# Kernel tuning notes

Measured on AMD Instinct MI355X. Metric: run time of the kernel, lower is better.

Reference implementation:

```python
import jax, jax.numpy as jnp
import numpy as np

TAU_MIN, TAU_MAX, TAU_SMALL, N_REF = 0.005, 0.1, 0.3, 4


def _l2norm(x, eps=1e-12):
    # matches torch F.normalize: x / max(||x||_2, eps)
    n = jnp.linalg.norm(x, axis=-1, keepdims=True)
    return x / jnp.maximum(n, eps)


def setup_inputs() -> dict:
    key = jax.random.key(0)
    k1, k2, k3 = jax.random.split(key, 3)
    B, C, H, W = 8, 384, 40, 40
    feats = jax.random.normal(k1, (B, C, H, W), dtype=jnp.float32)
    refs = jax.random.normal(k2, (N_REF, B, C, H, W), dtype=jnp.float32)
    sopm = jax.random.uniform(k3, (B, 1, 160, 160), dtype=jnp.float32)
    log_tau = jnp.array([np.log(0.03)], dtype=jnp.float32)
    alpha_raw = jnp.array([0.0], dtype=jnp.float32)
    return {"feats": feats, "refs": refs, "sopm": sopm,
            "log_tau": log_tau, "alpha_raw": alpha_raw}


def reference(feats, refs, sopm, log_tau, alpha_raw):
    B, C, H, W = feats.shape
    N = H * W
    # buffer contents and SOPM cache are detached in the torch module
    refs = jax.lax.stop_gradient(refs)
    sopm = jax.lax.stop_gradient(sopm)

    tau = jnp.clip(jnp.exp(log_tau[0]), TAU_MIN, TAU_MAX)
    alpha = jax.nn.sigmoid(alpha_raw[0])

    tokens = feats.reshape(B, C, N).transpose(0, 2, 1)   # [B, N, C]
    cur_n = _l2norm(tokens)

    n_ref = refs.shape[0]
    warped_sum = jnp.zeros_like(tokens)
    for r in range(n_ref):  # fixed small ref-frame loop (n_ref=4)
        ref_tok = refs[r].reshape(B, C, N).transpose(0, 2, 1)  # [B, N, C]
        ref_n = _l2norm(ref_tok)
        sim = jnp.einsum('bnc,bmc->bnm', cur_n, ref_n)          # cosine sims
        w = jax.nn.softmax(sim / tau, axis=-1)                  # [B, N, N]
        warped_sum = warped_sum + jnp.einsum('bnm,bmc->bnc', w, ref_tok)
    warped = warped_sum / n_ref

    # SOPM(t-1) -> bilinear resize (align_corners=False) -> threshold mask
    sopm_r = jax.image.resize(sopm, (B, 1, H, W), method='bilinear')
    mask = (sopm_r.reshape(B, 1, N).transpose(0, 2, 1) > TAU_SMALL).astype(feats.dtype)  # [B,N,1]

    alpha_eff = alpha  # full buffer: n_avail == n_ref
    fused = alpha_eff * warped + (1.0 - alpha_eff) * tokens
    enhanced = mask * fused + (1.0 - mask) * tokens
    return enhanced.transpose(0, 2, 1).reshape(B, C, H, W)
```

## Files before the change

### kernel.cpp

```cpp
#include <hip/hip_runtime.h>
#include <stdint.h>

#define B_  8
#define C_  384
#define N_  1600
#define R_  4
#define S_  160
#define HW_ 40

typedef float  f32x4  __attribute__((ext_vector_type(4)));
typedef __bf16 bf16x8 __attribute__((ext_vector_type(8)));
typedef long long i64t;

__device__ __forceinline__ unsigned short f2bf(float x){
  __bf16 h = (__bf16)x;
  return __builtin_bit_cast(unsigned short, h);
}
__device__ __forceinline__ float bf2f(unsigned short u){
  return __builtin_bit_cast(float, (uint32_t)u << 16);
}
__device__ __forceinline__ uint32_t pk_fp8x4(float a, float b, float c, float d){
  int lo = __builtin_amdgcn_cvt_pk_fp8_f32(a, b, 0, false);
  int hi = __builtin_amdgcn_cvt_pk_fp8_f32(c, d, 0, false);
  return (uint32_t)(lo & 0xffff) | ((uint32_t)hi << 16);
}

__device__ __forceinline__ void gload_lds16(const void* g, void* l){
  __builtin_amdgcn_global_load_lds(
      (const __attribute__((address_space(1))) uint32_t*)g,
      (__attribute__((address_space(3))) uint32_t*)l, 16, 0, 0);
}

__global__ void norm_kernel(const float* __restrict__ feats,
                            const float* __restrict__ refs,
                            float* __restrict__ invn){
  int gid = blockIdx.x * 256 + threadIdx.x;
  if (gid >= 16000) return;
  int mat = gid / 400;
  int n4  = (gid - mat * 400) * 4;
  const float* src = (mat < B_) ? (feats + (size_t)mat * C_ * N_)
                                : (refs  + (size_t)(mat - B_) * C_ * N_);
  f32x4 ss = {0.f,0.f,0.f,0.f};
  for (int c = 0; c < C_; ++c){
    f32x4 v = *(const f32x4*)(src + (size_t)c * N_ + n4);
    ss += v * v;
  }
  f32x4 r;
#pragma unroll
  for (int i = 0; i < 4; ++i) r[i] = 1.f / fmaxf(sqrtf(ss[i]), 1e-12f);
  *(f32x4*)(invn + (size_t)mat * N_ + n4) = r;
}

__global__ void prep_kernel(const float* __restrict__ feats,
                            const float* __restrict__ refs,
                            const float* __restrict__ invn,
                            unsigned char* __restrict__ Qb,
                            unsigned char* __restrict__ Kb,
                            unsigned short* __restrict__ Vb){
  int nt = blockIdx.x, ct = blockIdx.y, mat = blockIdx.z;
  __shared__ float tile[64][65];
  int t = threadIdx.x;
  bool isref = (mat >= B_);
  const float* src = isref ? refs  + (size_t)(mat - B_) * C_ * N_
                           : feats + (size_t)mat * C_ * N_;
#pragma unroll
  for (int i = 0; i < 4; ++i){
    int chunk = t + 256 * i;
    int cr = chunk >> 4, n4 = chunk & 15;
    size_t off = (size_t)(ct * 64 + cr) * N_ + nt * 64 + n4 * 4;
    float4 v = *(const float4*)(src + off);
    tile[cr][n4 * 4 + 0] = v.x;  tile[cr][n4 * 4 + 1] = v.y;
    tile[cr][n4 * 4 + 2] = v.z;  tile[cr][n4 * 4 + 3] = v.w;
    if (isref){
      ushort4 o;
      o.x = f2bf(v.x); o.y = f2bf(v.y); o.z = f2bf(v.z); o.w = f2bf(v.w);
      unsigned short* vdst = Vb + (size_t)(mat - B_) * C_ * N_;
      *(ushort4*)(vdst + off) = o;
    }
  }
  __syncthreads();
  unsigned char* dst = isref ? Kb + (size_t)(mat - B_) * N_ * C_
                             : Qb + (size_t)mat * N_ * C_;
  const float* ivp = invn + (size_t)mat * N_ + nt * 64;
#pragma unroll
  for (int i = 0; i < 4; ++i){
    int chunk = t + 256 * i;
    int nr = chunk >> 4, c4 = chunk & 15;
    float iv = ivp[nr];
    uint32_t pk = pk_fp8x4(tile[c4*4+0][nr] * iv, tile[c4*4+1][nr] * iv,
                           tile[c4*4+2][nr] * iv, tile[c4*4+3][nr] * iv);
    *(uint32_t*)(dst + (size_t)(nt*64+nr) * C_ + ct*64 + c4*4) = pk;
  }
}

__global__ void mask_kernel(const float* __restrict__ sopm,
                            float* __restrict__ maskp){
  int gid = blockIdx.x * 256 + threadIdx.x;
  int b = gid / N_, n = gid - b * N_;
  int oy = n / HW_, ox = n - oy * HW_;
  const float* sp = sopm + (size_t)b * S_ * S_;
  float cy = oy * 4 + 1.5f, cx = ox * 4 + 1.5f;
  int y0 = 4*oy - 2; if (y0 < 0) y0 = 0;
  int y1 = 4*oy + 5; if (y1 > S_-1) y1 = S_-1;
  int x0 = 4*ox - 2; if (x0 < 0) x0 = 0;
  int x1 = 4*ox + 5; if (x1 > S_-1) x1 = S_-1;
  float wsy = 0.f, wsx = 0.f;
  for (int j = y0; j <= y1; ++j) wsy += 1.f - fabsf(j - cy) * 0.25f;
  for (int j = x0; j <= x1; ++j) wsx += 1.f - fabsf(j - cx) * 0.25f;
  float acc = 0.f;
  for (int jy = y0; jy <= y1; ++jy){
    float wy = 1.f - fabsf(jy - cy) * 0.25f;
    float rs = 0.f;
    for (int jx = x0; jx <= x1; ++jx)
      rs += (1.f - fabsf(jx - cx) * 0.25f) * sp[jy * S_ + jx];
    acc += wy * rs;
  }
  float val = acc / (wsy * wsx);
  maskp[gid] = (val > 0.3f) ? 1.f : 0.f;
}

#define KB0_   0
#define KB1_   12288
#define VB_    24576
#define P_OFF  49152
#define LDS_SZ 53248

__global__ __launch_bounds__(256, 2) void attn_kernel(
    const unsigned char* __restrict__ Qb,
    const unsigned char* __restrict__ Kb,
    const unsigned short* __restrict__ Vb,
    const float* __restrict__ log_tau,
    unsigned short* __restrict__ Or)
{
  __shared__ __align__(16) char lds[LDS_SZ];
  int wg   = blockIdx.x;
  int orig = (wg & 7) * 100 + (wg >> 3);
  int qt   = orig % 25;
  int rb   = orig / 25;
  int b    = rb & 7;
  int tid  = threadIdx.x;
  int lane = tid & 63;
  int w    = tid >> 6;
  int mw   = w >> 1;
  int qw   = w & 1;
  int l15  = lane & 15;
  int lg   = lane >> 4;

  float tau = expf(log_tau[0]);
  tau = fminf(fmaxf(tau, 0.005f), 0.1f);
  float sc = 1.4426950408889634f / tau;

  i64t qreg[2][12];
#pragma unroll
  for (int qt2 = 0; qt2 < 2; ++qt2){
    const unsigned char* qp = Qb +
        ((size_t)b * N_ + qt * 64 + qw * 32 + qt2 * 16 + l15) * C_ + lg * 8;
#pragma unroll
    for (int ks = 0; ks < 12; ++ks)
      qreg[qt2][ks] = *(const i64t*)(qp + ks * 32);
  }

  f32x4 o[4][6];
#pragma unroll
  for (int i = 0; i < 4; ++i)
#pragma unroll
    for (int j = 0; j < 6; ++j) o[i][j] = (f32x4){0.f,0.f,0.f,0.f};
  float lsum0 = 0.f, lsum1 = 0.f;

  const unsigned char*  kmat = Kb + (size_t)rb * N_ * C_;
  const unsigned short* vmat = Vb + (size_t)rb * C_ * N_;
  char* Pb = lds + P_OFF;

  int koffB[3];
#pragma unroll
  for (int i = 0; i < 3; ++i){
    int L = (w * 3 + i) * 64 + lane;
    int m   = L / 24;
    int pos = L - m * 24;
    int cc  = (pos >> 3) * 8 + ((pos & 7) ^ (m & 7));
    koffB[i] = m * C_ + cc * 16;
  }
  int voff[6];
#pragma unroll
  for (int i = 0; i < 6; ++i){
    int chunk = (w * 6 + i) * 64 + lane;
    int line = chunk >> 3;
    int u    = (chunk & 7) ^ (line & 7);
    voff[i]  = (line * 2 + (u >> 2)) * N_ + (u & 3) * 8;
  }

  const int s_l  = (l15 >> 1) & 3;
  const int p_w0 = (qw*32      + l15) * 64 + (((2*mw + (lg >> 1)) ^ s_l) << 4) + (lg & 1) * 8;
  const int p_w1 = (qw*32 + 16 + l15) * 64 + (((2*mw + (lg >> 1)) ^ s_l) << 4) + (lg & 1) * 8;
  const int p_rc = ((lg ^ s_l) << 4) + l15 * 64;

  auto stageK = [&](int t, int buf){
    const unsigned char* kb = kmat + (size_t)t * 32 * C_;
    char* kdst = lds + (buf ? KB1_ : KB0_) + w * 3072;
#pragma unroll
    for (int i = 0; i < 3; ++i) gload_lds16(kb + koffB[i], kdst + i * 1024);
  };
  auto stageV = [&](int t){
    const unsigned short* vb = vmat + t * 32;
    char* vdst = lds + VB_ + w * 6144;
#pragma unroll
    for (int i = 0; i < 6; ++i) gload_lds16(vb + voff[i], vdst + i * 1024);
  };

  stageK(0, 0);
  stageV(0);
  stageK(1, 1);
  asm volatile("s_waitcnt vmcnt(9)" ::: "memory");
  __builtin_amdgcn_sched_barrier(0);
  __builtin_amdgcn_s_barrier();
  __builtin_amdgcn_sched_barrier(0);

  const int krow = (mw * 16 + l15);
  for (int mt = 0; mt < 50; ++mt){
    int cur = mt & 1;
    const char* kbR = lds + (cur ? KB1_ : KB0_);

    f32x4 s0 = {0.f,0.f,0.f,0.f}, s1 = {0.f,0.f,0.f,0.f};
    __builtin_amdgcn_s_setprio(1);
#pragma unroll
    for (int ks = 0; ks < 12; ++ks){
      int lc  = 2 * ks + (lg >> 1);
      int off = ((lc >> 3) * 8 + ((lc & 7) ^ (krow & 7))) * 16 + (lg & 1) * 8;
      i64t a = *(const i64t*)(kbR + krow * 384 + off);
      s0 = __builtin_amdgcn_mfma_f32_16x16x32_fp8_fp8(a, qreg[0][ks], s0, 0, 0, 0);
      s1 = __builtin_amdgcn_mfma_f32_16x16x32_fp8_fp8(a, qreg[1][ks], s1, 0, 0, 0);
    }
    __builtin_amdgcn_s_setprio(0);

    ushort4 pw0, pw1;
    {
      __bf16 h;
      float l0 = 0.f, l1 = 0.f;
      h = (__bf16)exp2f((s0[0]-1.f)*sc); l0 += (float)h; pw0.x = __builtin_bit_cast(unsigned short, h);
      h = (__bf16)exp2f((s0[1]-1.f)*sc); l0 += (float)h; pw0.y = __builtin_bit_cast(unsigned short, h);
      h = (__bf16)exp2f((s0[2]-1.f)*sc); l0 += (float)h; pw0.z = __builtin_bit_cast(unsigned short, h);
      h = (__bf16)exp2f((s0[3]-1.f)*sc); l0 += (float)h; pw0.w = __builtin_bit_cast(unsigned short, h);
      h = (__bf16)exp2f((s1[0]-1.f)*sc); l1 += (float)h; pw1.x = __builtin_bit_cast(unsigned short, h);
      h = (__bf16)exp2f((s1[1]-1.f)*sc); l1 += (float)h; pw1.y = __builtin_bit_cast(unsigned short, h);
      h = (__bf16)exp2f((s1[2]-1.f)*sc); l1 += (float)h; pw1.z = __builtin_bit_cast(unsigned short, h);
      h = (__bf16)exp2f((s1[3]-1.f)*sc); l1 += (float)h; pw1.w = __builtin_bit_cast(unsigned short, h);
      lsum0 += l0; lsum1 += l1;
    }
    *(ushort4*)(Pb + p_w0) = pw0;
    *(ushort4*)(Pb + p_w1) = pw1;
    asm volatile("s_waitcnt lgkmcnt(0) vmcnt(0)" ::: "memory");
    __builtin_amdgcn_sched_barrier(0);
    __builtin_amdgcn_s_barrier();
    __builtin_amdgcn_sched_barrier(0);

    int tk = (mt + 2 < 50) ? mt + 2 : mt;
    stageK(tk, cur);
    __builtin_amdgcn_sched_barrier(0);

    bf16x8 pa[4];
#pragma unroll
    for (int qf2 = 0; qf2 < 4; ++qf2)
      pa[qf2] = *(const bf16x8*)(Pb + qf2 * 1024 + p_rc);
    __builtin_amdgcn_s_setprio(1);
#pragma unroll
    for (int cf = 0; cf < 6; ++cf){
      int c  = w * 96 + cf * 16 + l15;
      int vo = (c >> 1) * 128 + (((lg | ((c & 1) << 2)) ^ ((c >> 1) & 7)) << 4);
      bf16x8 vf = *(const bf16x8*)(lds + VB_ + vo);
#pragma unroll
      for (int qf2 = 0; qf2 < 4; ++qf2)
        o[qf2][cf] = __builtin_amdgcn_mfma_f32_16x16x32_bf16(pa[qf2], vf, o[qf2][cf], 0, 0, 0);
    }
    __builtin_amdgcn_s_setprio(0);

    __builtin_amdgcn_sched_barrier(0);
    __builtin_amdgcn_s_barrier();
    __builtin_amdgcn_sched_barrier(0);

    int tv = (mt + 1 < 50) ? mt + 1 : 49;
    stageV(tv);
    __builtin_amdgcn_sched_barrier(0);
  }

  lsum0 += __shfl_xor(lsum0, 16, 64);
  lsum0 += __shfl_xor(lsum0, 32, 64);
  lsum1 += __shfl_xor(lsum1, 16, 64);
  lsum1 += __shfl_xor(lsum1, 32, 64);
  __syncthreads();
  float* lsh = (float*)lds;
  if (lg == 0){
    lsh[mw * 64 + qw * 32 + l15]      = lsum0;
    lsh[mw * 64 + qw * 32 + 16 + l15] = lsum1;
  }
  __syncthreads();
  float invl[4][4];
#pragma unroll
  for (int qf2 = 0; qf2 < 4; ++qf2)
#pragma unroll
    for (int rg = 0; rg < 4; ++rg){
      int q = qf2 * 16 + lg * 4 + rg;
      invl[qf2][rg] = 1.f / (lsh[q] + lsh[64 + q]);
    }

  int qbase = qt * 64;
  unsigned short* op = Or + ((size_t)rb * N_ + qbase) * C_ + w * 96 + l15;
#pragma unroll
  for (int qf2 = 0; qf2 < 4; ++qf2){
#pragma unroll
    for (int cf = 0; cf < 6; ++cf){
#pragma unroll
      for (int rg = 0; rg < 4; ++rg){
        int q = qf2 * 16 + lg * 4 + rg;
        op[(size_t)q * C_ + cf * 16] = f2bf(o[qf2][cf][rg] * invl[qf2][rg]);
      }
    }
  }
}

__global__ void combine_kernel(const unsigned short* __restrict__ Or,
                               const float* __restrict__ feats,
                               const float* __restrict__ maskp,
                               const float* __restrict__ alpha_raw,
                               float* __restrict__ out){
  int nt = blockIdx.x, ct = blockIdx.y, b = blockIdx.z;
  __shared__ float tile[64][65];
  float alpha = 1.f / (1.f + expf(-alpha_raw[0]));
  int t = threadIdx.x;
#pragma unroll
  for (int i = 0; i < 4; ++i){
    int chunk = t + 256 * i;
    int nr = chunk >> 4, c4 = chunk & 15;
    size_t base = ((size_t)b * N_ + nt * 64 + nr) * C_ + ct * 64 + c4 * 4;
    float4 s = {0.f,0.f,0.f,0.f};
#pragma unroll
    for (int r = 0; r < 4; ++r){
      ushort4 v = *(const ushort4*)(Or + (size_t)r * B_ * N_ * C_ + base);
      s.x += bf2f(v.x); s.y += bf2f(v.y); s.z += bf2f(v.z); s.w += bf2f(v.w);
    }
    tile[nr][c4*4+0] = s.x; tile[nr][c4*4+1] = s.y;
    tile[nr][c4*4+2] = s.z; tile[nr][c4*4+3] = s.w;
  }
  __syncthreads();
#pragma unroll
  for (int i = 0; i < 4; ++i){
    int chunk = t + 256 * i;
    int cr = chunk >> 4, n4 = chunk & 15;
    size_t fb = ((size_t)b * C_ + ct * 64 + cr) * N_ + nt * 64 + n4 * 4;
    float4 f  = *(const float4*)(feats + fb);
    float4 mk = *(const float4*)(maskp + (size_t)b * N_ + nt * 64 + n4 * 4);
    float4 ov;
    ov.x = f.x + mk.x * alpha * (tile[n4*4+0][cr] * 0.25f - f.x);
    ov.y = f.y + mk.y * alpha * (tile[n4*4+1][cr] * 0.25f - f.y);
    ov.z = f.z + mk.z * alpha * (tile[n4*4+2][cr] * 0.25f - f.z);
    ov.w = f.w + mk.w * alpha * (tile[n4*4+3][cr] * 0.25f - f.w);
    *(float4*)(out + fb) = ov;
  }
}

__global__ void poison_kernel(float* out, int n){
  int i = blockIdx.x * 256 + threadIdx.x;
  if (i < n) out[i] = 1.0e6f;
}

extern "C" void kernel_launch(void* const* d_in, const int* in_sizes, int n_in,
                              void* d_out, int out_size, void* d_ws, size_t ws_size,
                              hipStream_t stream){
  const float* feats     = (const float*)d_in[0];
  const float* refs      = (const float*)d_in[1];
  const float* sopm      = (const float*)d_in[2];
  const float* log_tau   = (const float*)d_in[3];
  const float* alpha_raw = (const float*)d_in[4];
  float* out = (float*)d_out;

  const size_t SZ_INVN = (size_t)(1 + R_) * B_ * N_ * 4;
  const size_t SZ_MASK = (size_t)B_ * N_ * 4;
  const size_t SZ_QB   = (size_t)B_ * N_ * C_;
  const size_t SZ_KB   = (size_t)R_ * B_ * N_ * C_;
  const size_t SZ_VB   = (size_t)R_ * B_ * N_ * C_ * 2;
  const size_t SZ_OR   = (size_t)R_ * B_ * N_ * C_ * 2;
  const size_t need = SZ_INVN + SZ_MASK + SZ_QB + SZ_KB + SZ_VB + SZ_OR;

  if (ws_size < need){
    poison_kernel<<<(out_size + 255) / 256, 256, 0, stream>>>(out, out_size);
    return;
  }
  char* ws = (char*)d_ws;
  float*          invn  = (float*)ws;
  float*          maskp = (float*)(ws + SZ_INVN);
  unsigned char*  Qb    = (unsigned char*)(ws + SZ_INVN + SZ_MASK);
  unsigned char*  Kb    = (unsigned char*)(ws + SZ_INVN + SZ_MASK + SZ_QB);
  unsigned short* Vb    = (unsigned short*)(ws + SZ_INVN + SZ_MASK + SZ_QB + SZ_KB);
  unsigned short* Or    = (unsigned short*)(ws + SZ_INVN + SZ_MASK + SZ_QB + SZ_KB + SZ_VB);

  norm_kernel   <<<63, 256, 0, stream>>>(feats, refs, invn);
  mask_kernel   <<<50, 256, 0, stream>>>(sopm, maskp);
  prep_kernel   <<<dim3(25, 6, 40), 256, 0, stream>>>(feats, refs, invn, Qb, Kb, Vb);
  attn_kernel   <<<800, 256, 0, stream>>>(Qb, Kb, Vb, log_tau, Or);
  combine_kernel<<<dim3(25, 6, 8), 256, 0, stream>>>(Or, feats, maskp, alpha_raw, out);
}
```

Before: 222.7 us.

## Split attention workgroup work across eight waves instead of four

Doubles the attention kernel's block size to 512 threads, so each wave handles 16 query rows for QK and 48 output channels for PV instead of 32 rows and 96 channels. The intent is to cut per-wave register pressure (accumulators and Q fragments) and add more waves to hide latency. In exchange, QK MFMA work is split finer with less K-fragment reuse per wave, only half the waves stage K, and the prologue now waits fully before issuing the second K prefetch. More barrier participants per iteration may add sync cost.

```diff
diff --git a/kernel.cpp b/kernel.cpp
--- a/kernel.cpp
+++ b/kernel.cpp
@@ -125,7 +125,7 @@
 #define P_OFF  49152
 #define LDS_SZ 53248
 
-__global__ __launch_bounds__(256, 2) void attn_kernel(
+__global__ __launch_bounds__(512, 2) void attn_kernel(
     const unsigned char* __restrict__ Qb,
     const unsigned char* __restrict__ Kb,
     const unsigned short* __restrict__ Vb,
@@ -141,8 +141,8 @@
   int tid  = threadIdx.x;
   int lane = tid & 63;
   int w    = tid >> 6;
-  int mw   = w >> 1;
-  int qw   = w & 1;
+  int mw   = w >> 2;
+  int qw   = w & 3;
   int l15  = lane & 15;
   int lg   = lane >> 4;
 
@@ -150,22 +150,21 @@
   tau = fminf(fmaxf(tau, 0.005f), 0.1f);
   float sc = 1.4426950408889634f / tau;
 
-  i64t qreg[2][12];
-#pragma unroll
-  for (int qt2 = 0; qt2 < 2; ++qt2){
+  i64t qreg[12];
+  {
     const unsigned char* qp = Qb +
-        ((size_t)b * N_ + qt * 64 + qw * 32 + qt2 * 16 + l15) * C_ + lg * 8;
+        ((size_t)b * N_ + qt * 64 + qw * 16 + l15) * C_ + lg * 8;
 #pragma unroll
     for (int ks = 0; ks < 12; ++ks)
-      qreg[qt2][ks] = *(const i64t*)(qp + ks * 32);
-  }
-
-  f32x4 o[4][6];
+      qreg[ks] = *(const i64t*)(qp + ks * 32);
+  }
+
+  f32x4 o[4][3];
 #pragma unroll
   for (int i = 0; i < 4; ++i)
 #pragma unroll
-    for (int j = 0; j < 6; ++j) o[i][j] = (f32x4){0.f,0.f,0.f,0.f};
-  float lsum0 = 0.f, lsum1 = 0.f;
+    for (int j = 0; j < 3; ++j) o[i][j] = (f32x4){0.f,0.f,0.f,0.f};
+  float lsum = 0.f;
 
   const unsigned char*  kmat = Kb + (size_t)rb * N_ * C_;
   const unsigned short* vmat = Vb + (size_t)rb * C_ * N_;
@@ -174,80 +173,75 @@
   int koffB[3];
 #pragma unroll
   for (int i = 0; i < 3; ++i){
-    int L = (w * 3 + i) * 64 + lane;
+    int L = ((w & 3) * 3 + i) * 64 + lane;
     int m   = L / 24;
     int pos = L - m * 24;
     int cc  = (pos >> 3) * 8 + ((pos & 7) ^ (m & 7));
     koffB[i] = m * C_ + cc * 16;
   }
-  int voff[6];
-#pragma unroll
-  for (int i = 0; i < 6; ++i){
-    int chunk = (w * 6 + i) * 64 + lane;
+  int voff[3];
+#pragma unroll
+  for (int i = 0; i < 3; ++i){
+    int chunk = (w * 3 + i) * 64 + lane;
     int line = chunk >> 3;
     int u    = (chunk & 7) ^ (line & 7);
     voff[i]  = (line * 2 + (u >> 2)) * N_ + (u & 3) * 8;
   }
 
   const int s_l  = (l15 >> 1) & 3;
-  const int p_w0 = (qw*32      + l15) * 64 + (((2*mw + (lg >> 1)) ^ s_l) << 4) + (lg & 1) * 8;
-  const int p_w1 = (qw*32 + 16 + l15) * 64 + (((2*mw + (lg >> 1)) ^ s_l) << 4) + (lg & 1) * 8;
+  const int p_w  = (qw*16 + l15) * 64 + (((mw*2 + (lg >> 1)) ^ s_l) << 4) + (lg & 1) * 8;
   const int p_rc = ((lg ^ s_l) << 4) + l15 * 64;
 
   auto stageK = [&](int t, int buf){
-    const unsigned char* kb = kmat + (size_t)t * 32 * C_;
-    char* kdst = lds + (buf ? KB1_ : KB0_) + w * 3072;
-#pragma unroll
-    for (int i = 0; i < 3; ++i) gload_lds16(kb + koffB[i], kdst + i * 1024);
+    if (w < 4){
+      const unsigned char* kb = kmat + (size_t)t * 32 * C_;
+      char* kdst = lds + (buf ? KB1_ : KB0_) + w * 3072;
+#pragma unroll
+      for (int i = 0; i < 3; ++i) gload_lds16(kb + koffB[i], kdst + i * 1024);
+    }
   };
   auto stageV = [&](int t){
     const unsigned short* vb = vmat + t * 32;
-    char* vdst = lds + VB_ + w * 6144;
-#pragma unroll
-    for (int i = 0; i < 6; ++i) gload_lds16(vb + voff[i], vdst + i * 1024);
+    char* vdst = lds + VB_ + w * 3072;
+#pragma unroll
+    for (int i = 0; i < 3; ++i) gload_lds16(vb + voff[i], vdst + i * 1024);
   };
 
   stageK(0, 0);
   stageV(0);
-  stageK(1, 1);
-  asm volatile("s_waitcnt vmcnt(9)" ::: "memory");
+  asm volatile("s_waitcnt vmcnt(0)" ::: "memory");
   __builtin_amdgcn_sched_barrier(0);
   __builtin_amdgcn_s_barrier();
   __builtin_amdgcn_sched_barrier(0);
+  stageK(1, 1);
 
   const int krow = (mw * 16 + l15);
   for (int mt = 0; mt < 50; ++mt){
     int cur = mt & 1;
     const char* kbR = lds + (cur ? KB1_ : KB0_);
 
-    f32x4 s0 = {0.f,0.f,0.f,0.f}, s1 = {0.f,0.f,0.f,0.f};
+    f32x4 s0 = {0.f,0.f,0.f,0.f};
     __builtin_amdgcn_s_setprio(1);
 #pragma unroll
     for (int ks = 0; ks < 12; ++ks){
       int lc  = 2 * ks + (lg >> 1);
       int off = ((lc >> 3) * 8 + ((lc & 7) ^ (krow & 7))) * 16 + (lg & 1) * 8;
       i64t a = *(const i64t*)(kbR + krow * 384 + off);
-      s0 = __builtin_amdgcn_mfma_f32_16x16x32_fp8_fp8(a, qreg[0][ks], s0, 0, 0, 0);
-      s1 = __builtin_amdgcn_mfma_f32_16x16x32_fp8_fp8(a, qreg[1][ks], s1, 0, 0, 0);
+      s0 = __builtin_amdgcn_mfma_f32_16x16x32_fp8_fp8(a, qreg[ks], s0, 0, 0, 0);
     }
     __builtin_amdgcn_s_setprio(0);
 
-    ushort4 pw0, pw1;
+    ushort4 pw;
     {
       __bf16 h;
-      float l0 = 0.f, l1 = 0.f;
-      h = (__bf16)exp2f((s0[0]-1.f)*sc); l0 += (float)h; pw0.x = __builtin_bit_cast(unsigned short, h);
-      h = (__bf16)exp2f((s0[1]-1.f)*sc); l0 += (float)h; pw0.y = __builtin_bit_cast(unsigned short, h);
-      h = (__bf16)exp2f((s0[2]-1.f)*sc); l0 += (float)h; pw0.z = __builtin_bit_cast(unsigned short, h);
-      h = (__bf16)exp2f((s0[3]-1.f)*sc); l0 += (float)h; pw0.w = __builtin_bit_cast(unsigned short, h);
-      h = (__bf16)exp2f((s1[0]-1.f)*sc); l1 += (float)h; pw1.x = __builtin_bit_cast(unsigned short, h);
-      h = (__bf16)exp2f((s1[1]-1.f)*sc); l1 += (float)h; pw1.y = __builtin_bit_cast(unsigned short, h);
-      h = (__bf16)exp2f((s1[2]-1.f)*sc); l1 += (float)h; pw1.z = __builtin_bit_cast(unsigned short, h);
-      h = (__bf16)exp2f((s1[3]-1.f)*sc); l1 += (float)h; pw1.w = __builtin_bit_cast(unsigned short, h);
-      lsum0 += l0; lsum1 += l1;
-    }
-    *(ushort4*)(Pb + p_w0) = pw0;
-    *(ushort4*)(Pb + p_w1) = pw1;
+      float l0 = 0.f;
+      h = (__bf16)exp2f((s0[0]-1.f)*sc); l0 += (float)h; pw.x = __builtin_bit_cast(unsigned short, h);
+      h = (__bf16)exp2f((s0[1]-1.f)*sc); l0 += (float)h; pw.y = __builtin_bit_cast(unsigned short, h);
+      h = (__bf16)exp2f((s0[2]-1.f)*sc); l0 += (float)h; pw.z = __builtin_bit_cast(unsigned short, h);
+      h = (__bf16)exp2f((s0[3]-1.f)*sc); l0 += (float)h; pw.w = __builtin_bit_cast(unsigned short, h);
+      lsum += l0;
+    }
+    *(ushort4*)(Pb + p_w) = pw;
     asm volatile("s_waitcnt lgkmcnt(0) vmcnt(0)" ::: "memory");
     __builtin_amdgcn_sched_barrier(0);
     __builtin_amdgcn_s_barrier();
@@ -263,8 +257,8 @@
       pa[qf2] = *(const bf16x8*)(Pb + qf2 * 1024 + p_rc);
     __builtin_amdgcn_s_setprio(1);
 #pragma unroll
-    for (int cf = 0; cf < 6; ++cf){
-      int c  = w * 96 + cf * 16 + l15;
+    for (int cf = 0; cf < 3; ++cf){
+      int c  = w * 48 + cf * 16 + l15;
       int vo = (c >> 1) * 128 + (((lg | ((c & 1) << 2)) ^ ((c >> 1) & 7)) << 4);
       bf16x8 vf = *(const bf16x8*)(lds + VB_ + vo);
 #pragma unroll
@@ -282,16 +276,11 @@
     __builtin_amdgcn_sched_barrier(0);
   }
 
-  lsum0 += __shfl_xor(lsum0, 16, 64);
-  lsum0 += __shfl_xor(lsum0, 32, 64);
-  lsum1 += __shfl_xor(lsum1, 16, 64);
-  lsum1 += __shfl_xor(lsum1, 32, 64);
+  lsum += __shfl_xor(lsum, 16, 64);
+  lsum += __shfl_xor(lsum, 32, 64);
   __syncthreads();
   float* lsh = (float*)lds;
-  if (lg == 0){
-    lsh[mw * 64 + qw * 32 + l15]      = lsum0;
-    lsh[mw * 64 + qw * 32 + 16 + l15] = lsum1;
-  }
+  if (lg == 0) lsh[mw * 64 + qw * 16 + l15] = lsum;
   __syncthreads();
   float invl[4][4];
 #pragma unroll
@@ -303,11 +292,11 @@
     }
 
   int qbase = qt * 64;
-  unsigned short* op = Or + ((size_t)rb * N_ + qbase) * C_ + w * 96 + l15;
+  unsigned short* op = Or + ((size_t)rb * N_ + qbase) * C_ + w * 48 + l15;
 #pragma unroll
   for (int qf2 = 0; qf2 < 4; ++qf2){
 #pragma unroll
-    for (int cf = 0; cf < 6; ++cf){
+    for (int cf = 0; cf < 3; ++cf){
 #pragma unroll
       for (int rg = 0; rg < 4; ++rg){
         int q = qf2 * 16 + lg * 4 + rg;
@@ -395,6 +384,6 @@
   norm_kernel   <<<63, 256, 0, stream>>>(feats, refs, invn);
   mask_kernel   <<<50, 256, 0, stream>>>(sopm, maskp);
   prep_kernel   <<<dim3(25, 6, 40), 256, 0, stream>>>(feats, refs, invn, Qb, Kb, Vb);
-  attn_kernel   <<<800, 256, 0, stream>>>(Qb, Kb, Vb, log_tau, Or);
+  attn_kernel   <<<800, 512, 0, stream>>>(Qb, Kb, Vb, log_tau, Or);
   combine_kernel<<<dim3(25, 6, 8), 256, 0, stream>>>(Or, feats, maskp, alpha_raw, out);
 }
```

After: 287.9 us. 29.3% more time.

## Fuse L2-norm computation into prep kernel, removing separate norm pass

Applied to the files above, without the earlier changes.

The standalone norm kernel, which read all feats and refs once to compute inverse L2 norms, is removed. The prep kernel now handles a 64-token by full-384-channel tile per block, accumulating sum-of-squares while it loads, and stages the data in LDS as bf16 before the normalized fp8 pack. This avoids a full extra read of the inputs and one launch, but the grid drops from 6000 to 1000 blocks with larger LDS use. Q/K are now quantized from bf16-rounded values instead of fp32, which adds a small precision loss.

```diff
diff --git a/kernel.cpp b/kernel.cpp
--- a/kernel.cpp
+++ b/kernel.cpp
@@ -31,65 +31,71 @@
       (__attribute__((address_space(3))) uint32_t*)l, 16, 0, 0);
 }
 
-__global__ void norm_kernel(const float* __restrict__ feats,
-                            const float* __restrict__ refs,
-                            float* __restrict__ invn){
-  int gid = blockIdx.x * 256 + threadIdx.x;
-  if (gid >= 16000) return;
-  int mat = gid / 400;
-  int n4  = (gid - mat * 400) * 4;
-  const float* src = (mat < B_) ? (feats + (size_t)mat * C_ * N_)
-                                : (refs  + (size_t)(mat - B_) * C_ * N_);
-  f32x4 ss = {0.f,0.f,0.f,0.f};
-  for (int c = 0; c < C_; ++c){
-    f32x4 v = *(const f32x4*)(src + (size_t)c * N_ + n4);
-    ss += v * v;
-  }
-  f32x4 r;
-#pragma unroll
-  for (int i = 0; i < 4; ++i) r[i] = 1.f / fmaxf(sqrtf(ss[i]), 1e-12f);
-  *(f32x4*)(invn + (size_t)mat * N_ + n4) = r;
-}
-
 __global__ void prep_kernel(const float* __restrict__ feats,
                             const float* __restrict__ refs,
-                            const float* __restrict__ invn,
                             unsigned char* __restrict__ Qb,
                             unsigned char* __restrict__ Kb,
                             unsigned short* __restrict__ Vb){
-  int nt = blockIdx.x, ct = blockIdx.y, mat = blockIdx.z;
-  __shared__ float tile[64][65];
+  int nt = blockIdx.x, mat = blockIdx.y;
+  __shared__ unsigned short tile[64][386];
+  __shared__ float ssp[64][17];
+  __shared__ float inv_sh[64];
   int t = threadIdx.x;
   bool isref = (mat >= B_);
   const float* src = isref ? refs  + (size_t)(mat - B_) * C_ * N_
                            : feats + (size_t)mat * C_ * N_;
-#pragma unroll
-  for (int i = 0; i < 4; ++i){
-    int chunk = t + 256 * i;
-    int cr = chunk >> 4, n4 = chunk & 15;
-    size_t off = (size_t)(ct * 64 + cr) * N_ + nt * 64 + n4 * 4;
-    float4 v = *(const float4*)(src + off);
-    tile[cr][n4 * 4 + 0] = v.x;  tile[cr][n4 * 4 + 1] = v.y;
-    tile[cr][n4 * 4 + 2] = v.z;  tile[cr][n4 * 4 + 3] = v.w;
-    if (isref){
+  int n4  = t & 15;
+  int crb = t >> 4;
+  float ss4[4] = {0.f, 0.f, 0.f, 0.f};
+#pragma unroll
+  for (int ct = 0; ct < 6; ++ct){
+#pragma unroll
+    for (int i = 0; i < 4; ++i){
+      int c = ct * 64 + crb + 16 * i;
+      size_t off = (size_t)c * N_ + nt * 64 + n4 * 4;
+      float4 v = *(const float4*)(src + off);
       ushort4 o;
       o.x = f2bf(v.x); o.y = f2bf(v.y); o.z = f2bf(v.z); o.w = f2bf(v.w);
-      unsigned short* vdst = Vb + (size_t)(mat - B_) * C_ * N_;
-      *(ushort4*)(vdst + off) = o;
-    }
+      if (isref){
+        unsigned short* vdst = Vb + (size_t)(mat - B_) * C_ * N_;
+        *(ushort4*)(vdst + off) = o;
+      }
+      tile[n4*4+0][c] = o.x;
+      tile[n4*4+1][c] = o.y;
+      tile[n4*4+2][c] = o.z;
+      tile[n4*4+3][c] = o.w;
+      ss4[0] += v.x * v.x;  ss4[1] += v.y * v.y;
+      ss4[2] += v.z * v.z;  ss4[3] += v.w * v.w;
+    }
+  }
+#pragma unroll
+  for (int j = 0; j < 4; ++j) ssp[n4*4+j][crb] = ss4[j];
+  __syncthreads();
+  if (t < 64){
+    float s = 0.f;
+#pragma unroll
+    for (int p = 0; p < 16; ++p) s += ssp[t][p];
+    inv_sh[t] = 1.f / fmaxf(sqrtf(s), 1e-12f);
   }
   __syncthreads();
   unsigned char* dst = isref ? Kb + (size_t)(mat - B_) * N_ * C_
                              : Qb + (size_t)mat * N_ * C_;
-  const float* ivp = invn + (size_t)mat * N_ + nt * 64;
 #pragma unroll
   for (int i = 0; i < 4; ++i){
-    int chunk = t + 256 * i;
-    int nr = chunk >> 4, c4 = chunk & 15;
-    float iv = ivp[nr];
-    uint32_t pk = pk_fp8x4(tile[c4*4+0][nr] * iv, tile[c4*4+1][nr] * iv,
-                           tile[c4*4+2][nr] * iv, tile[c4*4+3][nr] * iv);
-    *(uint32_t*)(dst + (size_t)(nt*64+nr) * C_ + ct*64 + c4*4) = pk;
+    int nr = (t >> 4) + 16 * i;
+    float iv = inv_sh[nr];
+    unsigned char* drow = dst + (size_t)(nt * 64 + nr) * C_;
+#pragma unroll
+    for (int ct = 0; ct < 6; ++ct){
+      int c0 = ct * 64 + (t & 15) * 4;
+      uint32_t a0 = *(const uint32_t*)(&tile[nr][c0]);
+      uint32_t a1 = *(const uint32_t*)(&tile[nr][c0 + 2]);
+      uint32_t pk = pk_fp8x4(bf2f((unsigned short)(a0 & 0xffff)) * iv,
+                             bf2f((unsigned short)(a0 >> 16))    * iv,
+                             bf2f((unsigned short)(a1 & 0xffff)) * iv,
+                             bf2f((unsigned short)(a1 >> 16))    * iv);
+      *(uint32_t*)(drow + c0) = pk;
+    }
   }
 }
 
@@ -372,29 +378,26 @@
   const float* alpha_raw = (const float*)d_in[4];
   float* out = (float*)d_out;
 
-  const size_t SZ_INVN = (size_t)(1 + R_) * B_ * N_ * 4;
   const size_t SZ_MASK = (size_t)B_ * N_ * 4;
   const size_t SZ_QB   = (size_t)B_ * N_ * C_;
   const size_t SZ_KB   = (size_t)R_ * B_ * N_ * C_;
   const size_t SZ_VB   = (size_t)R_ * B_ * N_ * C_ * 2;
   const size_t SZ_OR   = (size_t)R_ * B_ * N_ * C_ * 2;
-  const size_t need = SZ_INVN + SZ_MASK + SZ_QB + SZ_KB + SZ_VB + SZ_OR;
+  const size_t need = SZ_MASK + SZ_QB + SZ_KB + SZ_VB + SZ_OR;
 
   if (ws_size < need){
     poison_kernel<<<(out_size + 255) / 256, 256, 0, stream>>>(out, out_size);
     return;
   }
   char* ws = (char*)d_ws;
-  float*          invn  = (float*)ws;
-  float*          maskp = (float*)(ws + SZ_INVN);
-  unsigned char*  Qb    = (unsigned char*)(ws + SZ_INVN + SZ_MASK);
-  unsigned char*  Kb    = (unsigned char*)(ws + SZ_INVN + SZ_MASK + SZ_QB);
-  unsigned short* Vb    = (unsigned short*)(ws + SZ_INVN + SZ_MASK + SZ_QB + SZ_KB);
-  unsigned short* Or    = (unsigned short*)(ws + SZ_INVN + SZ_MASK + SZ_QB + SZ_KB + SZ_VB);
-
-  norm_kernel   <<<63, 256, 0, stream>>>(feats, refs, invn);
+  float*          maskp = (float*)ws;
+  unsigned char*  Qb    = (unsigned char*)(ws + SZ_MASK);
+  unsigned char*  Kb    = (unsigned char*)(ws + SZ_MASK + SZ_QB);
+  unsigned short* Vb    = (unsigned short*)(ws + SZ_MASK + SZ_QB + SZ_KB);
+  unsigned short* Or    = (unsigned short*)(ws + SZ_MASK + SZ_QB + SZ_KB + SZ_VB);
+
   mask_kernel   <<<50, 256, 0, stream>>>(sopm, maskp);
-  prep_kernel   <<<dim3(25, 6, 40), 256, 0, stream>>>(feats, refs, invn, Qb, Kb, Vb);
+  prep_kernel   <<<dim3(25, 40), 256, 0, stream>>>(feats, refs, Qb, Kb, Vb);
   attn_kernel   <<<800, 256, 0, stream>>>(Qb, Kb, Vb, log_tau, Or);
   combine_kernel<<<dim3(25, 6, 8), 256, 0, stream>>>(Or, feats, maskp, alpha_raw, out);
 }
```

After: 202.3 us, median of 2. -9.2%, faster.
